# Kernel tuning notes

Measured on AMD Instinct MI355X. Metric: run time of the kernel, lower is better.

## Reference

```python
import jax, jax.numpy as jnp
import numpy as np

TEMPERATURE = 8.0  # sqrt(head_dim=64)
NEG_INF = -1e9


def setup_inputs() -> dict:
    key = jax.random.key(0)
    k1, k2, k3, k4, k5 = jax.random.split(key, 5)
    B, H, S, D = 1, 8, 2048, 64
    q = jax.random.normal(k1, (B, H, S, D), dtype=jnp.float32)
    k = jax.random.normal(k2, (B, H, S, D), dtype=jnp.float32)
    v = jax.random.normal(k3, (B, H, S, D), dtype=jnp.float32)
    sph = jax.random.uniform(k4, (B, H, S, S), dtype=jnp.float32)
    mask = jax.random.randint(k5, (B, H, S, S), 0, 2, dtype=jnp.int32)
    return {"q": q, "k": k, "v": v, "sph": sph, "mask": mask}


def reference(q, k, v, sph, mask):
    # scores: [B,H,Sq,Sk]
    attn = jnp.einsum('bhqd,bhkd->bhqk', q / TEMPERATURE, k)
    attn = attn * sph                       # multiplicative bias
    attn = jnp.where(mask == 0, NEG_INF, attn)
    p_attn = jax.nn.softmax(attn, axis=-1)  # dropout p=0 -> identity
    out = jnp.einsum('bhqk,bhkd->bhqd', p_attn, v)
    return (out, p_attn)
```

## Files before the change

kernel.cpp:

```cpp
#include <hip/hip_runtime.h>

#define SLEN 2048
#define DIM  64
#define NH   8
#define TQ   16
#define NEG_INF -1e9f

typedef __attribute__((ext_vector_type(8))) short short8;
typedef __attribute__((ext_vector_type(4))) float f32x4;

__device__ inline unsigned short f2bf(float x) {
    unsigned u = __float_as_uint(x);
    u += 0x7fffu + ((u >> 16) & 1u);
    return (unsigned short)(u >> 16);
}
__device__ inline float bf2f(unsigned short b) {
    return __uint_as_float(((unsigned)b) << 16);
}

__global__ void conv_kernel(const float* __restrict__ k,
                            const float* __restrict__ v,
                            unsigned short* __restrict__ khi,
                            unsigned short* __restrict__ klo,
                            unsigned short* __restrict__ vt)
{
    int i = blockIdx.x * 256 + threadIdx.x;
    float x = k[i];
    unsigned short hi = f2bf(x);
    khi[i] = hi;
    klo[i] = f2bf(x - bf2f(hi));
    int s  = i & (SLEN - 1);
    int hd = i >> 11;
    int d  = hd & (DIM - 1);
    int hh = hd >> 6;
    vt[i] = f2bf(v[((size_t)(hh * SLEN + s)) * DIM + d]);
}

__global__ __launch_bounds__(512, 4)
void attn_mfma_kernel(const float* __restrict__ q,
                      const unsigned short* __restrict__ khi,
                      const unsigned short* __restrict__ klo,
                      const unsigned short* __restrict__ vt,
                      const float* __restrict__ sph,
                      const int*   __restrict__ mask,
                      float* __restrict__ out,
                      float* __restrict__ p_out)
{
    __shared__ unsigned short sP[TQ][SLEN + 8];
    __shared__ unsigned short sQhi[TQ][72];
    __shared__ unsigned short sQlo[TQ][72];
    __shared__ float sMax[TQ][8];
    __shared__ float sSum[TQ][8];
    __shared__ float sC[4][TQ][16];

    const int tid  = threadIdx.x;
    const int wave = tid >> 6;
    const int lane = tid & 63;
    const int quad = lane >> 4;
    const int l16  = lane & 15;
    const int bx   = blockIdx.x;
    const int h    = bx >> 7;
    const int qr0  = (bx & 127) * TQ;

    {
        int e = tid * 2;
        int r = e >> 6, d = e & 63;
        float2 qv = *(const float2*)(q + ((size_t)(h * SLEN + qr0 + r)) * DIM + d);
        unsigned short h0 = f2bf(qv.x), h1 = f2bf(qv.y);
        sQhi[r][d]     = h0;
        sQhi[r][d + 1] = h1;
        sQlo[r][d]     = f2bf(qv.x - bf2f(h0));
        sQlo[r][d + 1] = f2bf(qv.y - bf2f(h1));
    }
    __syncthreads();

    short8 ah0 = *(const short8*)(&sQhi[l16][quad * 8]);
    short8 ah1 = *(const short8*)(&sQhi[l16][32 + quad * 8]);
    short8 al0 = *(const short8*)(&sQlo[l16][quad * 8]);
    short8 al1 = *(const short8*)(&sQlo[l16][32 + quad * 8]);

    const int n0 = wave * 256;

    f32x4 c[16];
    #pragma unroll
    for (int t = 0; t < 16; ++t) c[t] = (f32x4){0.f, 0.f, 0.f, 0.f};

    #pragma unroll
    for (int t = 0; t < 16; ++t) {
        const size_t rowb = ((size_t)(h * SLEN + n0 + t * 16 + l16)) * DIM + quad * 8;
        short8 bh0 = *(const short8*)(khi + rowb);
        short8 bh1 = *(const short8*)(khi + rowb + 32);
        short8 bl0 = *(const short8*)(klo + rowb);
        short8 bl1 = *(const short8*)(klo + rowb + 32);
        c[t] = __builtin_amdgcn_mfma_f32_16x16x32_bf16(ah0, bh0, c[t], 0, 0, 0);
        c[t] = __builtin_amdgcn_mfma_f32_16x16x32_bf16(ah1, bh1, c[t], 0, 0, 0);
        c[t] = __builtin_amdgcn_mfma_f32_16x16x32_bf16(ah0, bl0, c[t], 0, 0, 0);
        c[t] = __builtin_amdgcn_mfma_f32_16x16x32_bf16(ah1, bl1, c[t], 0, 0, 0);
        c[t] = __builtin_amdgcn_mfma_f32_16x16x32_bf16(al0, bh0, c[t], 0, 0, 0);
        c[t] = __builtin_amdgcn_mfma_f32_16x16x32_bf16(al1, bh1, c[t], 0, 0, 0);
    }

    float rmax[4] = {-3.4e38f, -3.4e38f, -3.4e38f, -3.4e38f};
    #pragma unroll
    for (int t = 0; t < 16; ++t) {
        #pragma unroll
        for (int j = 0; j < 4; ++j) {
            const size_t idx = ((size_t)(h * SLEN) + qr0 + quad * 4 + j) * SLEN + n0 + t * 16 + l16;
            float s = c[t][j] * 0.125f * sph[idx];
            s = (mask[idx] == 0) ? NEG_INF : s;
            c[t][j] = s;
            rmax[j] = fmaxf(rmax[j], s);
        }
    }
    #pragma unroll
    for (int off = 1; off <= 8; off <<= 1) {
        #pragma unroll
        for (int j = 0; j < 4; ++j)
            rmax[j] = fmaxf(rmax[j], __shfl_xor(rmax[j], off));
    }
    if (l16 == 0) {
        #pragma unroll
        for (int j = 0; j < 4; ++j) sMax[quad * 4 + j][wave] = rmax[j];
    }
    __syncthreads();

    float M[4];
    #pragma unroll
    for (int j = 0; j < 4; ++j) {
        float m = sMax[quad * 4 + j][0];
        #pragma unroll
        for (int w = 1; w < 8; ++w) m = fmaxf(m, sMax[quad * 4 + j][w]);
        M[j] = m;
    }

    float rsum[4] = {0.f, 0.f, 0.f, 0.f};
    #pragma unroll
    for (int t = 0; t < 16; ++t) {
        #pragma unroll
        for (int j = 0; j < 4; ++j) {
            float e = __expf(c[t][j] - M[j]);
            c[t][j] = e;
            rsum[j] += e;
        }
    }
    #pragma unroll
    for (int off = 1; off <= 8; off <<= 1) {
        #pragma unroll
        for (int j = 0; j < 4; ++j)
            rsum[j] += __shfl_xor(rsum[j], off);
    }
    if (l16 == 0) {
        #pragma unroll
        for (int j = 0; j < 4; ++j) sSum[quad * 4 + j][wave] = rsum[j];
    }
    __syncthreads();

    float inv[4];
    #pragma unroll
    for (int j = 0; j < 4; ++j) {
        float s = 0.f;
        #pragma unroll
        for (int w = 0; w < 8; ++w) s += sSum[quad * 4 + j][w];
        inv[j] = 1.0f / s;
    }

    #pragma unroll
    for (int t = 0; t < 16; ++t) {
        #pragma unroll
        for (int j = 0; j < 4; ++j) {
            const int row = quad * 4 + j;
            const int col = n0 + t * 16 + l16;
            const size_t idx = ((size_t)(h * SLEN) + qr0 + row) * SLEN + col;
            float p = c[t][j] * inv[j];
            p_out[idx] = p;
            sP[row][col] = f2bf(p);
        }
    }
    __syncthreads();

    const int ntile = wave & 3;
    const int khalf = wave >> 2;
    f32x4 o = (f32x4){0.f, 0.f, 0.f, 0.f};
    const unsigned short* vb = vt + ((size_t)(h * DIM + ntile * 16 + l16)) * SLEN
                                  + khalf * 1024 + quad * 8;
    #pragma unroll 8
    for (int s = 0; s < 32; ++s) {
        short8 a = *(const short8*)(&sP[l16][khalf * 1024 + s * 32 + quad * 8]);
        short8 b = *(const short8*)(vb + s * 32);
        o = __builtin_amdgcn_mfma_f32_16x16x32_bf16(a, b, o, 0, 0, 0);
    }
    if (wave >= 4) {
        #pragma unroll
        for (int j = 0; j < 4; ++j) sC[ntile][quad * 4 + j][l16] = o[j];
    }
    __syncthreads();
    if (wave < 4) {
        #pragma unroll
        for (int j = 0; j < 4; ++j) {
            float r = o[j] + sC[ntile][quad * 4 + j][l16];
            out[((size_t)(h * SLEN) + qr0 + quad * 4 + j) * DIM + ntile * 16 + l16] = r;
        }
    }
}

extern "C" void kernel_launch(void* const* d_in, const int* in_sizes, int n_in,
                              void* d_out, int out_size, void* d_ws, size_t ws_size,
                              hipStream_t stream) {
    const float* q    = (const float*)d_in[0];
    const float* k    = (const float*)d_in[1];
    const float* v    = (const float*)d_in[2];
    const float* sph  = (const float*)d_in[3];
    const int*   mask = (const int*)d_in[4];
    float* out   = (float*)d_out;
    float* p_out = out + (size_t)NH * SLEN * DIM;

    const size_t nkv = (size_t)NH * SLEN * DIM;
    unsigned short* khi = (unsigned short*)d_ws;
    unsigned short* klo = khi + nkv;
    unsigned short* vt  = klo + nkv;

    hipLaunchKernelGGL(conv_kernel, dim3(nkv / 256), dim3(256), 0, stream,
                       k, v, khi, klo, vt);
    hipLaunchKernelGGL(attn_mfma_kernel, dim3(NH * (SLEN / TQ)), dim3(512), 0, stream,
                       q, khi, klo, vt, sph, mask, out, p_out);
}
```

Measured before the change: 470.8 us.

## Split and vectorize K/V conversion, batch nontemporal sph/mask loads, relax launch bounds

The combined conversion kernel is split into a float4-vectorized K hi/lo split and a V transpose kernel that goes through LDS, so V reads are coalesced instead of strided. In the attention kernel, sph and mask loads are issued in batches of 32 per half using nontemporal loads, raising memory-level parallelism. The p_attn and out writes become nontemporal stores. Launch bounds drop from 4 to 2 blocks per SM to allow more registers for the batched loads, at the cost of occupancy and one extra kernel launch.

```diff
diff --git a/kernel.cpp b/kernel.cpp
--- a/kernel.cpp
+++ b/kernel.cpp
@@ -8,47 +8,75 @@
 
 typedef __attribute__((ext_vector_type(8))) short short8;
 typedef __attribute__((ext_vector_type(4))) float f32x4;
-
-__device__ inline unsigned short f2bf(float x) {
+typedef unsigned short ushort;
+
+__device__ inline ushort f2bf(float x) {
     unsigned u = __float_as_uint(x);
     u += 0x7fffu + ((u >> 16) & 1u);
-    return (unsigned short)(u >> 16);
-}
-__device__ inline float bf2f(unsigned short b) {
+    return (ushort)(u >> 16);
+}
+__device__ inline float bf2f(ushort b) {
     return __uint_as_float(((unsigned)b) << 16);
 }
 
-__global__ void conv_kernel(const float* __restrict__ k,
-                            const float* __restrict__ v,
-                            unsigned short* __restrict__ khi,
-                            unsigned short* __restrict__ klo,
-                            unsigned short* __restrict__ vt)
+__global__ __launch_bounds__(256)
+void convk_kernel(const float* __restrict__ k,
+                  ushort* __restrict__ khi, ushort* __restrict__ klo)
 {
-    int i = blockIdx.x * 256 + threadIdx.x;
-    float x = k[i];
-    unsigned short hi = f2bf(x);
-    khi[i] = hi;
-    klo[i] = f2bf(x - bf2f(hi));
-    int s  = i & (SLEN - 1);
-    int hd = i >> 11;
-    int d  = hd & (DIM - 1);
-    int hh = hd >> 6;
-    vt[i] = f2bf(v[((size_t)(hh * SLEN + s)) * DIM + d]);
-}
-
-__global__ __launch_bounds__(512, 4)
+    int i4 = blockIdx.x * 256 + threadIdx.x;
+    float4 x = ((const float4*)k)[i4];
+    ushort h0 = f2bf(x.x), h1 = f2bf(x.y), h2 = f2bf(x.z), h3 = f2bf(x.w);
+    ushort4 hi = {h0, h1, h2, h3};
+    ushort4 lo = {f2bf(x.x - bf2f(h0)), f2bf(x.y - bf2f(h1)),
+                  f2bf(x.z - bf2f(h2)), f2bf(x.w - bf2f(h3))};
+    ((ushort4*)khi)[i4] = hi;
+    ((ushort4*)klo)[i4] = lo;
+}
+
+__global__ __launch_bounds__(256)
+void convv_kernel(const float* __restrict__ v, ushort* __restrict__ vt)
+{
+    __shared__ ushort sT[64][70];
+    const int h  = blockIdx.x >> 5;
+    const int st = blockIdx.x & 31;
+    const int t  = threadIdx.x;
+    {
+        const int r0 = t >> 4;
+        const int c  = (t & 15) * 4;
+        #pragma unroll
+        for (int rr = r0; rr < 64; rr += 16) {
+            float4 x = *(const float4*)(v + ((size_t)(h * SLEN + st * 64 + rr)) * DIM + c);
+            sT[c + 0][rr] = f2bf(x.x);
+            sT[c + 1][rr] = f2bf(x.y);
+            sT[c + 2][rr] = f2bf(x.z);
+            sT[c + 3][rr] = f2bf(x.w);
+        }
+    }
+    __syncthreads();
+    {
+        const int d  = t >> 2;
+        const int s0 = (t & 3) * 16;
+        short8 a = *(const short8*)(&sT[d][s0]);
+        short8 b = *(const short8*)(&sT[d][s0 + 8]);
+        ushort* dst = vt + ((size_t)(h * DIM + d)) * SLEN + st * 64 + s0;
+        *(short8*)(dst)     = a;
+        *(short8*)(dst + 8) = b;
+    }
+}
+
+__global__ __launch_bounds__(512, 2)
 void attn_mfma_kernel(const float* __restrict__ q,
-                      const unsigned short* __restrict__ khi,
-                      const unsigned short* __restrict__ klo,
-                      const unsigned short* __restrict__ vt,
+                      const ushort* __restrict__ khi,
+                      const ushort* __restrict__ klo,
+                      const ushort* __restrict__ vt,
                       const float* __restrict__ sph,
                       const int*   __restrict__ mask,
                       float* __restrict__ out,
                       float* __restrict__ p_out)
 {
-    __shared__ unsigned short sP[TQ][SLEN + 8];
-    __shared__ unsigned short sQhi[TQ][72];
-    __shared__ unsigned short sQlo[TQ][72];
+    __shared__ ushort sP[TQ][SLEN + 8];
+    __shared__ ushort sQhi[TQ][72];
+    __shared__ ushort sQlo[TQ][72];
     __shared__ float sMax[TQ][8];
     __shared__ float sSum[TQ][8];
     __shared__ float sC[4][TQ][16];
@@ -66,7 +94,7 @@
         int e = tid * 2;
         int r = e >> 6, d = e & 63;
         float2 qv = *(const float2*)(q + ((size_t)(h * SLEN + qr0 + r)) * DIM + d);
-        unsigned short h0 = f2bf(qv.x), h1 = f2bf(qv.y);
+        ushort h0 = f2bf(qv.x), h1 = f2bf(qv.y);
         sQhi[r][d]     = h0;
         sQhi[r][d + 1] = h1;
         sQlo[r][d]     = f2bf(qv.x - bf2f(h0));
@@ -100,14 +128,27 @@
         c[t] = __builtin_amdgcn_mfma_f32_16x16x32_bf16(al1, bh1, c[t], 0, 0, 0);
     }
 
+    size_t rowb[4];
+    #pragma unroll
+    for (int j = 0; j < 4; ++j)
+        rowb[j] = ((size_t)(h * SLEN) + qr0 + quad * 4 + j) * SLEN + n0 + l16;
+
     float rmax[4] = {-3.4e38f, -3.4e38f, -3.4e38f, -3.4e38f};
     #pragma unroll
-    for (int t = 0; t < 16; ++t) {
-        #pragma unroll
-        for (int j = 0; j < 4; ++j) {
-            const size_t idx = ((size_t)(h * SLEN) + qr0 + quad * 4 + j) * SLEN + n0 + t * 16 + l16;
-            float s = c[t][j] * 0.125f * sph[idx];
-            s = (mask[idx] == 0) ? NEG_INF : s;
+    for (int half = 0; half < 2; ++half) {
+        float sv[32];
+        int   mv[32];
+        #pragma unroll
+        for (int u = 0; u < 32; ++u) {
+            const int t = half * 8 + (u >> 2), j = u & 3;
+            sv[u] = __builtin_nontemporal_load(sph  + rowb[j] + t * 16);
+            mv[u] = __builtin_nontemporal_load(mask + rowb[j] + t * 16);
+        }
+        #pragma unroll
+        for (int u = 0; u < 32; ++u) {
+            const int t = half * 8 + (u >> 2), j = u & 3;
+            float s = c[t][j] * 0.125f * sv[u];
+            s = (mv[u] == 0) ? NEG_INF : s;
             c[t][j] = s;
             rmax[j] = fmaxf(rmax[j], s);
         }
@@ -170,9 +211,8 @@
         for (int j = 0; j < 4; ++j) {
             const int row = quad * 4 + j;
             const int col = n0 + t * 16 + l16;
-            const size_t idx = ((size_t)(h * SLEN) + qr0 + row) * SLEN + col;
             float p = c[t][j] * inv[j];
-            p_out[idx] = p;
+            __builtin_nontemporal_store(p, p_out + rowb[j] + t * 16);
             sP[row][col] = f2bf(p);
         }
     }
@@ -181,8 +221,8 @@
     const int ntile = wave & 3;
     const int khalf = wave >> 2;
     f32x4 o = (f32x4){0.f, 0.f, 0.f, 0.f};
-    const unsigned short* vb = vt + ((size_t)(h * DIM + ntile * 16 + l16)) * SLEN
-                                  + khalf * 1024 + quad * 8;
+    const ushort* vb = vt + ((size_t)(h * DIM + ntile * 16 + l16)) * SLEN
+                          + khalf * 1024 + quad * 8;
     #pragma unroll 8
     for (int s = 0; s < 32; ++s) {
         short8 a = *(const short8*)(&sP[l16][khalf * 1024 + s * 32 + quad * 8]);
@@ -198,7 +238,8 @@
         #pragma unroll
         for (int j = 0; j < 4; ++j) {
             float r = o[j] + sC[ntile][quad * 4 + j][l16];
-            out[((size_t)(h * SLEN) + qr0 + quad * 4 + j) * DIM + ntile * 16 + l16] = r;
+            __builtin_nontemporal_store(
+                r, out + ((size_t)(h * SLEN) + qr0 + quad * 4 + j) * DIM + ntile * 16 + l16);
         }
     }
 }
@@ -215,12 +256,14 @@
     float* p_out = out + (size_t)NH * SLEN * DIM;
 
     const size_t nkv = (size_t)NH * SLEN * DIM;
-    unsigned short* khi = (unsigned short*)d_ws;
-    unsigned short* klo = khi + nkv;
-    unsigned short* vt  = klo + nkv;
-
-    hipLaunchKernelGGL(conv_kernel, dim3(nkv / 256), dim3(256), 0, stream,
-                       k, v, khi, klo, vt);
+    ushort* khi = (ushort*)d_ws;
+    ushort* klo = khi + nkv;
+    ushort* vt  = klo + nkv;
+
+    hipLaunchKernelGGL(convk_kernel, dim3(nkv / 4 / 256), dim3(256), 0, stream,
+                       k, khi, klo);
+    hipLaunchKernelGGL(convv_kernel, dim3(NH * (SLEN / 64)), dim3(256), 0, stream,
+                       v, vt);
     hipLaunchKernelGGL(attn_mfma_kernel, dim3(NH * (SLEN / TQ)), dim3(512), 0, stream,
                        q, khi, klo, vt, sph, mask, out, p_out);
 }
```

Result: faster. 417.6 us (-11.3%).
